# Performance work log

Hardware: AMD Instinct MI355X
Metric: run time of the kernel (lower is better)

The kernel has to match this reference:

```python
import jax, jax.numpy as jnp
import numpy as np

NEG_SLOPE = 0.2
EPS = 1e-9


def setup_inputs() -> dict:
    key = jax.random.key(0)
    ks = jax.random.split(key, 6)
    B, N, E, H, F = 2, 40000, 640000, 4, 32
    X = jax.random.normal(ks[0], (B, N, H, F), dtype=jnp.float32)
    A_self = jax.random.normal(ks[1], (H, F), dtype=jnp.float32)
    A_adjc = jax.random.normal(ks[2], (H, F), dtype=jnp.float32)
    targets = jax.random.randint(ks[3], (B, E), 0, N, dtype=jnp.int32)
    sources = jax.random.randint(ks[4], (B, E), 0, N, dtype=jnp.int32)
    degree = jax.random.uniform(ks[5], (B, E), dtype=jnp.float32)
    return {"X": X, "A_self": A_self, "A_adjc": A_adjc, "degree": degree,
            "targets": targets, "sources": sources, "N": N}


def reference(X, A_self, A_adjc, degree, targets, sources, N):
    # X: [B, N, H, F]; targets/sources: [B, E]
    # per-node attention logits: [B, N, H]
    e_self = jnp.einsum("bnhf,hf->bnh", X, A_self)
    e_adjc = jnp.einsum("bnhf,hf->bnh", X, A_adjc)
    # gather to edges: [B, E, H]
    es = jnp.take_along_axis(e_self, targets[:, :, None], axis=1)
    ea = jnp.take_along_axis(e_adjc, sources[:, :, None], axis=1)
    e = jax.nn.leaky_relu(es + ea, negative_slope=NEG_SLOPE)

    seg_max = jax.vmap(lambda v, i: jax.ops.segment_max(v, i, num_segments=N))
    seg_sum = jax.vmap(lambda v, i: jax.ops.segment_sum(v, i, num_segments=N))

    # exact normalization from source: exp(e - seg_max(e)), then divide by
    # seg_max of the exponentials (+eps), both gathered back to edges.
    m1 = jnp.take_along_axis(seg_max(e, targets), targets[:, :, None], axis=1)
    e = jnp.exp(e - m1)
    m2 = jnp.take_along_axis(seg_max(e, targets), targets[:, :, None], axis=1)
    attn = (e / (m2 + EPS))[..., None]  # [B, E, H, 1]; dropout omitted (eval)

    # message passing: gather source features, weight, scatter-sum to targets
    msg = jnp.take_along_axis(X, sources[:, :, None, None], axis=1) * attn  # [B,E,H,F]
    out = seg_sum(msg, targets)  # [B, N, H, F]
    return out
```

## Files before the change

### kernel.cpp

```cpp
#include <hip/hip_runtime.h>
#include <stdint.h>

#define BB     2
#define NNODE  40000
#define NEDGE  640000
#define NH     4
#define NF     32
#define NHF    128
#define SEGN   (BB * NNODE)
#define GEDGE  (BB * NEDGE)
#define EC     32
#define SLOT   48

#define W      512
#define NBK_B  79
#define NBK    (BB * NBK_B)
#define CAP    9216
#define BLK_E  2048
#define NBLKA  (GEDGE / BLK_E)

static constexpr float NEG_SLOPE = 0.2f;
static constexpr float NEG_BIG   = -3.4e38f;

__global__ void prep_k(const float* __restrict__ X,
                       const float* __restrict__ As,
                       const float* __restrict__ Aa,
                       float* __restrict__ S, float* __restrict__ A,
                       unsigned* __restrict__ cursor) {
    int idx = blockIdx.x * blockDim.x + threadIdx.x;
    if (idx < NBK) cursor[idx] = 0u;
    if (idx >= SEGN * NH) return;
    int h = idx & (NH - 1);
    const float4* xv = (const float4*)(X + (size_t)idx * NF);
    const float4* sv = (const float4*)(As + h * NF);
    const float4* av = (const float4*)(Aa + h * NF);
    float s = 0.f, a = 0.f;
#pragma unroll
    for (int i = 0; i < 8; ++i) {
        float4 x = xv[i];
        float4 ws = sv[i];
        float4 wa = av[i];
        s += x.x * ws.x + x.y * ws.y + x.z * ws.z + x.w * ws.w;
        a += x.x * wa.x + x.y * wa.y + x.z * wa.z + x.w * wa.w;
    }
    S[idx] = s;
    A[idx] = a;
}

__global__ __launch_bounds__(256) void binA_k(const int* __restrict__ tg,
                                              const int* __restrict__ sc,
                                              unsigned* __restrict__ cursor,
                                              unsigned* __restrict__ pairs) {
    __shared__ unsigned hist[NBK];
    __shared__ unsigned lofs[NBK];
    __shared__ unsigned gofs[NBK];
    __shared__ unsigned staged[BLK_E];
    __shared__ unsigned char sbk[BLK_E];
    int t = threadIdx.x;
    int base = blockIdx.x * BLK_E;
    for (int i = t; i < NBK; i += 256) hist[i] = 0u;
    __syncthreads();

    unsigned pr[8];
    unsigned short pbk[8], plp[8];
#pragma unroll
    for (int k = 0; k < 8; ++k) {
        int e = base + k * 256 + t;
        int tgv = tg[e], scv = sc[e];
        int b = (e >= NEDGE) ? 1 : 0;
        unsigned bk = (unsigned)(b * NBK_B + (tgv >> 9));
        pr[k]  = ((unsigned)(tgv & (W - 1)) << 16) | (unsigned)scv;
        pbk[k] = (unsigned short)bk;
        plp[k] = (unsigned short)atomicAdd(&hist[bk], 1u);
    }
    __syncthreads();
    if (t == 0) {
        unsigned run = 0;
        for (int i = 0; i < NBK; ++i) { lofs[i] = run; run += hist[i]; }
    }
    __syncthreads();
    if (t < NBK && hist[t] > 0u)
        gofs[t] = atomicAdd(&cursor[t], hist[t]);
    __syncthreads();
#pragma unroll
    for (int k = 0; k < 8; ++k) {
        unsigned j = lofs[pbk[k]] + plp[k];
        staged[j] = pr[k];
        sbk[j] = (unsigned char)pbk[k];
    }
    __syncthreads();
    for (int j = t; j < BLK_E; j += 256) {
        unsigned bk = sbk[j];
        unsigned dst = gofs[bk] + ((unsigned)j - lofs[bk]);
        if (dst < CAP)
            pairs[(size_t)bk * CAP + dst] = staged[j];
    }
}

__global__ __launch_bounds__(256) void binB_k(const unsigned* __restrict__ cursor,
                                              const unsigned* __restrict__ pairs,
                                              unsigned short* __restrict__ srt,
                                              unsigned* __restrict__ deg) {
    __shared__ unsigned short loc[W * SLOT];
    __shared__ unsigned dloc[W];
    int t = threadIdx.x;
    int gbk = blockIdx.x;
    int b = gbk / NBK_B;
    int bkloc = gbk - b * NBK_B;
    int node0 = b * NNODE + bkloc * W;
    int wEff = min(W, NNODE - bkloc * W);
    for (int i = t; i < W; i += 256) dloc[i] = 0u;
    __syncthreads();
    int nE = (int)min(cursor[gbk], (unsigned)CAP);
    const unsigned* pb = pairs + (size_t)gbk * CAP;
    for (int j = t; j < nE; j += 256) {
        unsigned p = pb[j];
        unsigned tl = p >> 16;
        unsigned pos = atomicAdd(&dloc[tl], 1u);
        if (pos < SLOT)
            loc[tl * SLOT + pos] = (unsigned short)(p & 0xFFFFu);
    }
    __syncthreads();
    unsigned* srt32 = (unsigned*)(srt + (size_t)node0 * SLOT);
    const unsigned* loc32 = (const unsigned*)loc;
    int n32 = wEff * SLOT / 2;
    for (int i = t; i < n32; i += 256) srt32[i] = loc32[i];
    for (int i = t; i < wEff; i += 256) deg[node0 + i] = dloc[i];
}

__global__ __launch_bounds__(NHF) void gather_k(
        const float* __restrict__ X, const float* __restrict__ S,
        const float* __restrict__ A, const unsigned* __restrict__ deg,
        const unsigned short* __restrict__ srt, float* __restrict__ OUT) {
    int node = blockIdx.x;
    int t = threadIdx.x;
    int h4 = t & 3;
    int er = t >> 2;
    int h  = t >> 5;
    int dg = min((int)deg[node], SLOT);
    int bbase = (node >= NNODE) ? NNODE : 0;
    size_t beg = (size_t)node * SLOT;

    __shared__ float lred[NHF];
    __shared__ float lmh[NH];
    __shared__ float lw[EC * NH];
    __shared__ int   lsb[EC];

    float sh4 = S[node * NH + h4];
    float acc = 0.f;
    if (t < NH) lmh[t] = NEG_BIG;
    __syncthreads();

    for (int c = 0; c < dg; c += EC) {
        int e = c + er;
        int sb = 0;
        float v = NEG_BIG;
        if (e < dg) {
            sb = bbase + (int)srt[beg + e];
            v = sh4 + A[sb * NH + h4];
            v = v > 0.f ? v : NEG_SLOPE * v;
        }
        lred[t] = v;
        __syncthreads();
        for (int s = 64; s >= 4; s >>= 1) {
            if (t < s) lred[t] = fmaxf(lred[t], lred[t + s]);
            __syncthreads();
        }
        if (t < NH) {
            float mold = lmh[t];
            float mnew = fmaxf(mold, lred[t]);
            lmh[t] = mnew;
            lred[64 + t] = (mold == NEG_BIG) ? 0.f : __expf(mold - mnew);
        }
        __syncthreads();
        acc *= lred[64 + h];
        lw[er * NH + h4] = (e < dg) ? __expf(v - lmh[h4]) : 0.f;
        if (h4 == 0) lsb[er] = sb;
        __syncthreads();

        int cend = min(EC, dg - c);
#pragma unroll 4
        for (int e2 = 0; e2 < cend; ++e2) {
            float w  = lw[e2 * NH + h];
            int  sb2 = lsb[e2];
            acc += X[(size_t)sb2 * NHF + t] * w;
        }
        __syncthreads();
    }
    OUT[(size_t)node * NHF + t] = acc;
}

extern "C" void kernel_launch(void* const* d_in, const int* in_sizes, int n_in,
                              void* d_out, int out_size, void* d_ws, size_t ws_size,
                              hipStream_t stream) {
    const float* X  = (const float*)d_in[0];
    const float* As = (const float*)d_in[1];
    const float* Aa = (const float*)d_in[2];
    const int* tg = (const int*)d_in[4];
    const int* sc = (const int*)d_in[5];
    float* OUT = (float*)d_out;

    char* ws = (char*)d_ws;
    float*          S      = (float*)ws;
    float*          A      = (float*)(ws + 1280000);
    unsigned*       deg    = (unsigned*)(ws + 2560000);
    unsigned*       cursor = (unsigned*)(ws + 2880000);
    unsigned*       pairs  = (unsigned*)(ws + 2880640);
    unsigned short* srt    = (unsigned short*)(ws + 8705152);

    const int nlog = SEGN * NH;
    prep_k<<<(nlog + 255) / 256, 256, 0, stream>>>(X, As, Aa, S, A, cursor);
    binA_k<<<NBLKA, 256, 0, stream>>>(tg, sc, cursor, pairs);
    binB_k<<<NBK, 256, 0, stream>>>(cursor, pairs, srt, deg);
    gather_k<<<SEGN, NHF, 0, stream>>>(X, S, A, deg, srt, OUT);
}
```

Baseline: 238.2 us.

## Rewrite gather kernel as single-wavefront with shuffle reductions and float2 accumulation

The gather kernel now runs one 64-lane wavefront per node instead of 128 threads. The shared-memory tree max-reduction and broadcasts of weights and source indices are replaced by cross-lane shuffles, which removes every __syncthreads. Each lane accumulates two features through float2 loads, and the edge chunk size drops from 32 to 16 to fit the wavefront. The online rescaling is reorganised into per-lane running maxima. Each lane now does more serial work per edge, in exchange for losing the barrier and LDS overhead.

```diff
diff --git a/kernel.cpp b/kernel.cpp
--- a/kernel.cpp
+++ b/kernel.cpp
@@ -9,7 +9,7 @@
 #define NHF    128
 #define SEGN   (BB * NNODE)
 #define GEDGE  (BB * NEDGE)
-#define EC     32
+#define EC     16
 #define SLOT   48
 
 #define W      512
@@ -128,66 +128,57 @@
     for (int i = t; i < wEff; i += 256) deg[node0 + i] = dloc[i];
 }
 
-__global__ __launch_bounds__(NHF) void gather_k(
+__global__ __launch_bounds__(64) void gather_k(
         const float* __restrict__ X, const float* __restrict__ S,
         const float* __restrict__ A, const unsigned* __restrict__ deg,
         const unsigned short* __restrict__ srt, float* __restrict__ OUT) {
     int node = blockIdx.x;
     int t = threadIdx.x;
-    int h4 = t & 3;
-    int er = t >> 2;
-    int h  = t >> 5;
+    int hs = t & 3;
+    int es = t >> 2;
+    int ha = t >> 4;
     int dg = min((int)deg[node], SLOT);
     int bbase = (node >= NNODE) ? NNODE : 0;
     size_t beg = (size_t)node * SLOT;
 
-    __shared__ float lred[NHF];
-    __shared__ float lmh[NH];
-    __shared__ float lw[EC * NH];
-    __shared__ int   lsb[EC];
-
-    float sh4 = S[node * NH + h4];
-    float acc = 0.f;
-    if (t < NH) lmh[t] = NEG_BIG;
-    __syncthreads();
+    float sh = S[node * NH + hs];
+    float m_st = NEG_BIG;
+    float m_ac = NEG_BIG;
+    float ax = 0.f, ay = 0.f;
 
     for (int c = 0; c < dg; c += EC) {
-        int e = c + er;
-        int sb = 0;
+        int e = c + es;
+        int sb = bbase;
         float v = NEG_BIG;
         if (e < dg) {
             sb = bbase + (int)srt[beg + e];
-            v = sh4 + A[sb * NH + h4];
+            v = sh + A[sb * NH + hs];
             v = v > 0.f ? v : NEG_SLOPE * v;
         }
-        lred[t] = v;
-        __syncthreads();
-        for (int s = 64; s >= 4; s >>= 1) {
-            if (t < s) lred[t] = fmaxf(lred[t], lred[t + s]);
-            __syncthreads();
+        float m = v;
+        m = fmaxf(m, __shfl_xor(m, 4));
+        m = fmaxf(m, __shfl_xor(m, 8));
+        m = fmaxf(m, __shfl_xor(m, 16));
+        m = fmaxf(m, __shfl_xor(m, 32));
+        m_st = fmaxf(m_st, m);
+        float w = (e < dg) ? __expf(v - m_st) : 0.f;
+        float ma_new = fmaxf(m_ac, __shfl(m, ha));
+        float r = __expf(m_ac - ma_new);
+        m_ac = ma_new;
+        ax *= r; ay *= r;
+
+        int cend = min(EC, dg - c);
+#pragma unroll 8
+        for (int e2 = 0; e2 < cend; ++e2) {
+            float we  = __shfl(w, 4 * e2 + ha);
+            int   sbe = __shfl(sb, 4 * e2);
+            const float2 x = *(const float2*)(X + (size_t)sbe * NHF + 2 * t);
+            ax += x.x * we;
+            ay += x.y * we;
         }
-        if (t < NH) {
-            float mold = lmh[t];
-            float mnew = fmaxf(mold, lred[t]);
-            lmh[t] = mnew;
-            lred[64 + t] = (mold == NEG_BIG) ? 0.f : __expf(mold - mnew);
-        }
-        __syncthreads();
-        acc *= lred[64 + h];
-        lw[er * NH + h4] = (e < dg) ? __expf(v - lmh[h4]) : 0.f;
-        if (h4 == 0) lsb[er] = sb;
-        __syncthreads();
-
-        int cend = min(EC, dg - c);
-#pragma unroll 4
-        for (int e2 = 0; e2 < cend; ++e2) {
-            float w  = lw[e2 * NH + h];
-            int  sb2 = lsb[e2];
-            acc += X[(size_t)sb2 * NHF + t] * w;
-        }
-        __syncthreads();
-    }
-    OUT[(size_t)node * NHF + t] = acc;
+    }
+    float2* o = (float2*)(OUT + (size_t)node * NHF + 2 * t);
+    *o = make_float2(ax, ay);
 }
 
 extern "C" void kernel_launch(void* const* d_in, const int* in_sizes, int n_in,
@@ -212,5 +203,5 @@
     prep_k<<<(nlog + 255) / 256, 256, 0, stream>>>(X, As, Aa, S, A, cursor);
     binA_k<<<NBLKA, 256, 0, stream>>>(tg, sc, cursor, pairs);
     binB_k<<<NBK, 256, 0, stream>>>(cursor, pairs, srt, deg);
-    gather_k<<<SEGN, NHF, 0, stream>>>(X, S, A, deg, srt, OUT);
-}
+    gather_k<<<SEGN, 64, 0, stream>>>(X, S, A, deg, srt, OUT);
+}
```

After: 238.1 us. Within noise of the previous version (-0.1%).
